# Kernel optimization log

Measured on AMD Instinct MI355X. Metric: run time of the kernel, lower is better.

## Reference

```python
import jax, jax.numpy as jnp
import numpy as np

SD = 64      # state_dim
EMO = 16     # emo_dim
D = SD + EMO # fractal node dim
C = SD       # quantum in/out channels
E = SD * 5   # MHA embed dim (320)
NH = 4       # MHA heads
HD = E // NH
F = D * 5    # flattened fractal node state
LIGHT = 500.0


def setup_inputs() -> dict:
    key = jax.random.key(0)
    ks = iter(jax.random.split(key, 48))
    def n(shape, s=0.02):
        return jax.random.normal(next(ks), shape, dtype=jnp.float32) * s
    return dict(
        node_states=jax.random.normal(next(ks), (27, SD, 5), dtype=jnp.float32),
        hist_state=jax.random.normal(next(ks), (27, SD, 5), dtype=jnp.float32),
        # CausalDiscoveryLayer params
        granger_W=n((2 * SD * 5, 1)), granger_b=jnp.zeros((1,), jnp.float32),
        mha_in_W=n((3 * E, E)), mha_in_b=jnp.zeros((3 * E,), jnp.float32),
        mha_out_W=n((E, E)), mha_out_b=jnp.zeros((E,), jnp.float32),
        # QuantumEntangledGNN params
        q_real=n((27, C), 0.01), q_imag=n((27, C), 0.01),
        ent_W1=n((2 * C, 64)), ent_b1=jnp.zeros((64,), jnp.float32),
        ent_W2=n((64, C)), ent_b2=jnp.zeros((C,), jnp.float32),
        meas_W=n((2 * C, C * 5)), meas_b=jnp.zeros((C * 5,), jnp.float32),
        # FractalGNN (depth 2, 27-ary): 729 leaves, 27 mid, 1 root
        leaf_states=n((729, D, 5), 0.01),
        mid_states=n((27, D, 5), 0.01),
        root_state=n((D, 5), 0.01),
        mid_agg_W=n((27, 27 * F, F)), mid_agg_b=jnp.zeros((27, F), jnp.float32),
        root_agg_W=n((27 * F, F)), root_agg_b=jnp.zeros((F,), jnp.float32),
        mid_up_W1=n((27, 2 * F, 64)), mid_up_b1=jnp.zeros((27, 64), jnp.float32),
        mid_up_W2=n((27, 64, F)), mid_up_b2=jnp.zeros((27, F), jnp.float32),
        root_up_W1=n((2 * F, 64)), root_up_b1=jnp.zeros((64,), jnp.float32),
        root_up_W2=n((64, F)), root_up_b2=jnp.zeros((F,), jnp.float32),
    )


def _forward(node_states, hist_state, granger_W, granger_b, mha_in_W, mha_in_b,
             mha_out_W, mha_out_b, q_real, q_imag, ent_W1, ent_b1, ent_W2, ent_b2,
             meas_W, meas_b, leaf_states, mid_states, root_state, mid_agg_W,
             mid_agg_b, root_agg_W, root_agg_b, mid_up_W1, mid_up_b1, mid_up_W2,
             mid_up_b2, root_up_W1, root_up_b1, root_up_W2, root_up_b2):
    # ---- CausalDiscoveryLayer ----
    h = hist_state.reshape(27, SD * 5)   # historical_states[-1][j].view(-1)
    x = node_states.reshape(27, SD * 5)  # node_states[i].view(-1)
    # pred_input[i, j] = cat(hist[j], node[i]) -> granger test, all 27x27 pairs
    pred = jnp.concatenate([
        jnp.broadcast_to(h[None, :, :], (27, 27, SD * 5)),
        jnp.broadcast_to(x[:, None, :], (27, 27, SD * 5))], axis=-1)
    scores = jax.nn.sigmoid(pred @ granger_W + granger_b)[..., 0]
    # .item() in original detaches -> stop_gradient; diagonal stays zero
    causal_adj = jax.lax.stop_gradient(scores * (1.0 - jnp.eye(27, dtype=scores.dtype)))
    hertz_w = jnp.clip(jnp.float32(LIGHT / 1000.0), 0.1, 1.0)
    qkv = x @ mha_in_W.T + mha_in_b
    q, k, v = jnp.split(qkv, 3, axis=-1)
    qh = q.reshape(27, NH, HD).transpose(1, 0, 2)  # [h, s, d]
    kh = k.reshape(27, NH, HD).transpose(1, 0, 2)
    vh = v.reshape(27, NH, HD).transpose(1, 0, 2)
    attn = jax.nn.softmax(jnp.einsum('hqd,hkd->hqk', qh, kh) / jnp.float32(HD) ** 0.5, axis=-1)
    o = jnp.einsum('hqk,hkd->hqd', attn, vh).transpose(1, 0, 2).reshape(27, E)
    attended = ((o @ mha_out_W.T + mha_out_b) * hertz_w).reshape(27, SD, 5)

    # ---- QuantumEntangledGNN (351 unordered pairs i<j) ----
    iu, ju = np.triu_indices(27, 1)
    comb = jnp.concatenate([q_real[iu], q_real[ju]], axis=-1)       # [351, 2C]
    ent = jax.nn.relu(comb @ ent_W1 + ent_b1) @ ent_W2 + ent_b2     # [351, C]
    s = q_real.sum(axis=1)
    coupling = jnp.exp(-jnp.abs(s[iu] - s[ju]) / (LIGHT + 1e-6))
    avg_ent = (ent * coupling[:, None]).mean(axis=0)                # [C]
    qr = q_real + avg_ent[None, :]
    qi = q_imag + avg_ent[None, :]
    measured = (jnp.concatenate([qr, qi], axis=-1) @ meas_W + meas_b).reshape(3, 3, 3, C, 5)

    # ---- FractalGNN: leaves are passthrough; 27 mid nodes update, then root ----
    child_flat = leaf_states.reshape(27, 27 * F)  # each mid node's 27 leaf children
    agg = jnp.einsum('nij,ni->nj', mid_agg_W, child_flat) + mid_agg_b  # [27, F]
    comb_m = jnp.concatenate([mid_states.reshape(27, F), agg], axis=-1)
    hid = jax.nn.relu(jnp.einsum('nij,ni->nj', mid_up_W1, comb_m) + mid_up_b1)
    upd = jnp.einsum('nij,ni->nj', mid_up_W2, hid) + mid_up_b2
    new_mid = mid_states + upd.reshape(27, D, 5)
    cf = new_mid.reshape(27 * F)
    agg_r = cf @ root_agg_W + root_agg_b
    comb_r = jnp.concatenate([root_state.reshape(F), agg_r], axis=-1)
    new_root = root_state + (jax.nn.relu(comb_r @ root_up_W1 + root_up_b1) @ root_up_W2 + root_up_b2).reshape(D, 5)

    return causal_adj, attended, measured, new_root


def reference(node_states, hist_state, granger_W, granger_b, mha_in_W, mha_in_b,
              mha_out_W, mha_out_b, q_real, q_imag, ent_W1, ent_b1, ent_W2, ent_b2,
              meas_W, meas_b, leaf_states, mid_states, root_state, mid_agg_W,
              mid_agg_b, root_agg_W, root_agg_b, mid_up_W1, mid_up_b1, mid_up_W2,
              mid_up_b2, root_up_W1, root_up_b1, root_up_W2, root_up_b2):
    return _forward(node_states, hist_state, granger_W, granger_b, mha_in_W,
                    mha_in_b, mha_out_W, mha_out_b, q_real, q_imag, ent_W1, ent_b1,
                    ent_W2, ent_b2, meas_W, meas_b, leaf_states, mid_states,
                    root_state, mid_agg_W, mid_agg_b, root_agg_W, root_agg_b,
                    mid_up_W1, mid_up_b1, mid_up_W2, mid_up_b2, root_up_W1,
                    root_up_b1, root_up_W2, root_up_b2)
```

## Files before the change

kernel.cpp:

```cpp
#include <hip/hip_runtime.h>
#include <math.h>

typedef float v4f __attribute__((ext_vector_type(4)));

#define SD 64
#define CC 64
#define EE 320
#define NS 27
#define NPAIR 351

#define NCHUNK 54
#define AGG_BLKS (27 * NCHUNK)

#define WS_QKV   0
#define WS_ENT   25920
#define WS_MIDP  48384
#define WS_CF    1214784
#define WS_ROOTP 1225584
#define WS_HPM   1268784
#define WS_HPR   1275696
#define WS_CTR   1275968


__device__ void dev_mid_agg(int blk, const float* __restrict__ W,
                            const float* __restrict__ leaf, float* __restrict__ partial) {
    __shared__ float c_l[200];
    int n = blk / NCHUNK, chunk = blk % NCHUNK;
    int t = threadIdx.x;
    if (t < 200) c_l[t] = leaf[n * 10800 + chunk * 200 + t];
    __syncthreads();
    if (t < 200) {
        int rp = t / 100, j4 = t % 100;
        const v4f* Wr = (const v4f*)(W + (size_t)(n * 10800 + chunk * 200) * 400);
        v4f acc = (v4f)(0.0f);
        #pragma unroll 16
        for (int rr = 0; rr < 100; ++rr) {
            int r = 2 * rr + rp;
            v4f w = __builtin_nontemporal_load(&Wr[(size_t)r * 100 + j4]);
            acc += c_l[r] * w;
        }
        ((v4f*)(partial + (size_t)(blk * 2 + rp) * 400))[j4] = acc;
    }
}

__device__ void dev_granger(int blk, const float* __restrict__ x, const float* __restrict__ h,
                            const float* __restrict__ gW, const float* __restrict__ gb,
                            float* __restrict__ out) {
    int idx = blk * 256 + threadIdx.x;
    if (idx >= NS * NS) return;
    int i = idx / NS, j = idx % NS;
    const float* hr = h + j * 320;
    const float* xr = x + i * 320;
    float acc = gb[0];
    for (int k = 0; k < 320; ++k) acc += hr[k] * gW[k] + xr[k] * gW[320 + k];
    float sig = 1.0f / (1.0f + expf(-acc));
    out[idx] = (i == j) ? 0.0f : sig;
}

__device__ void dev_qkv(int blk, const float* __restrict__ x, const float* __restrict__ W,
                        const float* __restrict__ b, float* __restrict__ qkv) {
    int idx = blk * 256 + threadIdx.x;
    if (idx >= NS * 960) return;
    int i = idx / 960, c = idx % 960;
    const float4* xr = (const float4*)(x + i * 320);
    const float4* wr = (const float4*)(W + (size_t)c * 320);
    float acc = b[c];
    #pragma unroll 8
    for (int k = 0; k < 80; ++k) {
        float4 a = xr[k], w = wr[k];
        acc += a.x * w.x + a.y * w.y + a.z * w.z + a.w * w.w;
    }
    qkv[idx] = acc;
}

__device__ void dev_ent(int blk, const float* __restrict__ q_real,
                        const float* __restrict__ W1, const float* __restrict__ b1,
                        const float* __restrict__ W2, const float* __restrict__ b2,
                        float* __restrict__ ent_scaled) {
    __shared__ float comb[2][128];
    __shared__ float hid[2][64];
    int t = threadIdx.x;
    int sub = t >> 7, lt = t & 127;
    int p = blk * 2 + sub;
    bool pv = (p < NPAIR);
    bool valid = pv && (lt < 64);
    int i = 0, jj = 0;
    if (pv) {
        int rem = p;
        while (rem >= 26 - i) { rem -= 26 - i; ++i; }
        jj = i + 1 + rem;
    }
    float qa = 0.f, qb = 0.f;
    if (valid) { qa = q_real[i * CC + lt]; qb = q_real[jj * CC + lt]; }
    float sa = qa, sb = qb;
    #pragma unroll
    for (int off = 32; off; off >>= 1) { sa += __shfl_xor(sa, off); sb += __shfl_xor(sb, off); }
    float coupling = expf(-fabsf(sa - sb) / (500.0f + 1e-6f));
    if (valid) { comb[sub][lt] = qa; comb[sub][64 + lt] = qb; }
    __syncthreads();
    if (valid) {
        float hs = b1[lt];
        for (int ii = 0; ii < 128; ++ii) hs += comb[sub][ii] * W1[ii * 64 + lt];
        hid[sub][lt] = fmaxf(hs, 0.0f);
    }
    __syncthreads();
    if (valid) {
        float e = b2[lt];
        for (int k = 0; k < 64; ++k) e += hid[sub][k] * W2[k * 64 + lt];
        ent_scaled[p * 64 + lt] = e * coupling;
    }
}

__global__ __launch_bounds__(256) void k_stage1(
    const float* __restrict__ mid_agg_W, const float* __restrict__ leaf,
    const float* __restrict__ node, const float* __restrict__ hist,
    const float* __restrict__ gW, const float* __restrict__ gb,
    const float* __restrict__ mha_in_W, const float* __restrict__ mha_in_b,
    const float* __restrict__ q_real,
    const float* __restrict__ ent_W1, const float* __restrict__ ent_b1,
    const float* __restrict__ ent_W2, const float* __restrict__ ent_b2,
    float* __restrict__ mid_partial, float* __restrict__ out_causal,
    float* __restrict__ qkv, float* __restrict__ ent_scaled,
    int* __restrict__ ctrs) {
    int blk = blockIdx.x;
    if (blk == 0 && threadIdx.x >= 224) ctrs[threadIdx.x - 224] = 0;
    if (blk < AGG_BLKS)            dev_mid_agg(blk, mid_agg_W, leaf, mid_partial);
    else if (blk < AGG_BLKS + 3)   dev_granger(blk - AGG_BLKS, node, hist, gW, gb, out_causal);
    else if (blk < AGG_BLKS + 105) dev_qkv(blk - AGG_BLKS - 3, node, mha_in_W, mha_in_b, qkv);
    else                           dev_ent(blk - AGG_BLKS - 105, q_real, ent_W1, ent_b1, ent_W2, ent_b2, ent_scaled);
}


__device__ void dev_attn(int blk, const float* __restrict__ qkv, float* __restrict__ o) {
    int h = blk / NS, q = blk % NS;
    int t = threadIdx.x;
    __shared__ float sc[NS];
    __shared__ float at[NS];
    if (t < NS) {
        const float* qrow = qkv + q * 960 + h * 80;
        const float* krow = qkv + t * 960 + EE + h * 80;
        float s = 0.0f;
        for (int d = 0; d < 80; ++d) s += qrow[d] * krow[d];
        sc[t] = s * 0.1118033988749895f;
    }
    __syncthreads();
    if (t < NS) {
        float m = -1e30f;
        for (int s2 = 0; s2 < NS; ++s2) m = fmaxf(m, sc[s2]);
        float sum = 0.0f;
        for (int s2 = 0; s2 < NS; ++s2) sum += expf(sc[s2] - m);
        at[t] = expf(sc[t] - m) / sum;
    }
    __syncthreads();
    if (t < 80) {
        float acc = 0.0f;
        for (int s2 = 0; s2 < NS; ++s2) acc += at[s2] * qkv[s2 * 960 + 2 * EE + h * 80 + t];
        o[q * EE + h * 80 + t] = acc;
    }
}

__device__ void dev_avg(const float* __restrict__ ent_scaled, float* __restrict__ avg) {
    __shared__ float aacc[8][64];
    int t = threadIdx.x;
    int col = t & 63, grp = t >> 6;
    float s = 0.0f;
    for (int p = grp; p < NPAIR; p += 8) s += ent_scaled[p * 64 + col];
    aacc[grp][col] = s;
    __syncthreads();
    if (t < 64) {
        float a = 0.0f;
        #pragma unroll
        for (int g = 0; g < 8; ++g) a += aacc[g][t];
        avg[t] = a / (float)NPAIR;
    }
}

__device__ void dev_mid_up(int rel, const float* __restrict__ partial, const float* __restrict__ agg_b,
                           const float* __restrict__ mid_states,
                           const float* __restrict__ W1, const float* __restrict__ b1,
                           const float* __restrict__ W2, const float* __restrict__ b2,
                           float* __restrict__ cf, float* __restrict__ hpm, int* __restrict__ ctrs) {
    int n = rel >> 2, p = rel & 3;
    __shared__ float combq[200];
    __shared__ float hp8[8][64];
    __shared__ float hid[64];
    __shared__ int flag;
    int t = threadIdx.x;
    if (p < 2) {
        if (t < 200) combq[t] = mid_states[n * 400 + p * 200 + t];
    } else {
        int j0 = (p - 2) * 200;
        if (t < 200) {
            float a = agg_b[n * 400 + j0 + t];
            const float* pp = partial + (size_t)(n * 108) * 400 + j0 + t;
            #pragma unroll 12
            for (int s = 0; s < 108; ++s) a += pp[s * 400];
            combq[t] = a;
        }
    }
    __syncthreads();
    {
        int h = t & 63, g = t >> 6;
        const float* w1 = W1 + (size_t)n * 51200 + (size_t)(p * 200) * 64;
        float hs = 0.0f;
        #pragma unroll 5
        for (int i = g * 25; i < g * 25 + 25; ++i) hs += combq[i] * w1[i * 64 + h];
        hp8[g][h] = hs;
    }
    __syncthreads();
    if (t < 64) {
        float hs = 0.0f;
        #pragma unroll
        for (int g = 0; g < 8; ++g) hs += hp8[g][t];
        hpm[(n * 4 + p) * 64 + t] = hs;
    }
    __syncthreads();
    if (t == 0) {
        int old = __hip_atomic_fetch_add(&ctrs[n], 1, __ATOMIC_ACQ_REL, __HIP_MEMORY_SCOPE_AGENT);
        flag = (old == 3);
    }
    __syncthreads();
    if (flag) {
        if (t < 64) {
            float hs = b1[n * 64 + t];
            #pragma unroll
            for (int pq = 0; pq < 4; ++pq) hs += hpm[(n * 4 + pq) * 64 + t];
            hid[t] = fmaxf(hs, 0.0f);
        }
        __syncthreads();
        const float* w2 = W2 + (size_t)n * 25600;
        if (t < 400) {
            float u = b2[n * 400 + t];
            #pragma unroll 8
            for (int k = 0; k < 64; ++k) u += hid[k] * w2[k * 400 + t];
            cf[n * 400 + t] = mid_states[n * 400 + t] + u;
        }
    }
}

__global__ __launch_bounds__(512) void k_stage2(
    const float* __restrict__ qkv, float* __restrict__ o,
    const float* __restrict__ ent_scaled, float* __restrict__ avg,
    const float* __restrict__ mid_partial, const float* __restrict__ mid_agg_b,
    const float* __restrict__ mid_states,
    const float* __restrict__ mid_up_W1, const float* __restrict__ mid_up_b1,
    const float* __restrict__ mid_up_W2, const float* __restrict__ mid_up_b2,
    float* __restrict__ cf, float* __restrict__ hpm, int* __restrict__ ctrs) {
    int blk = blockIdx.x;
    if (blk < 108)       dev_attn(blk, qkv, o);
    else if (blk == 108) dev_avg(ent_scaled, avg);
    else                 dev_mid_up(blk - 109, mid_partial, mid_agg_b, mid_states,
                                    mid_up_W1, mid_up_b1, mid_up_W2, mid_up_b2, cf, hpm, ctrs);
}


__device__ void dev_proj(int blk, const float* __restrict__ o, const float* __restrict__ W,
                         const float* __restrict__ b, float* __restrict__ outp) {
    int idx = blk * 512 + threadIdx.x;
    if (idx >= NS * EE) return;
    int i = idx / EE, c = idx % EE;
    const float4* orow = (const float4*)(o + i * EE);
    const float4* wr = (const float4*)(W + (size_t)c * EE);
    float acc = b[c];
    #pragma unroll 8
    for (int k = 0; k < 80; ++k) {
        float4 a = orow[k], w = wr[k];
        acc += a.x * w.x + a.y * w.y + a.z * w.z + a.w * w.w;
    }
    outp[idx] = 0.5f * acc;
}

__device__ void dev_measured(int blk, const float* __restrict__ q_real, const float* __restrict__ q_imag,
                             const float* __restrict__ avg, const float* __restrict__ W,
                             const float* __restrict__ b, float* __restrict__ out) {
    int idx = blk * 512 + threadIdx.x;
    if (idx >= NS * EE) return;
    int i = idx / EE, c = idx % EE;
    float acc = b[c];
    #pragma unroll 8
    for (int k = 0; k < 64; ++k) {
        float a = avg[k];
        acc += (q_real[i * 64 + k] + a) * W[k * EE + c];
        acc += (q_imag[i * 64 + k] + a) * W[(64 + k) * EE + c];
    }
    out[idx] = acc;
}

__device__ void dev_rootagg(int chunk, const float* __restrict__ W, const float* __restrict__ cf,
                            float* __restrict__ partial_r) {
    __shared__ float racc[5][400];
    int t = threadIdx.x;
    int rp = t / 100, j4 = t % 100;
    if (rp < 5) {
        const float* c = cf + chunk * 100;
        const v4f* Wr = (const v4f*)W + (size_t)(chunk * 100) * 100;
        v4f acc = (v4f)(0.0f);
        #pragma unroll
        for (int rr = 0; rr < 20; ++rr) {
            int r = 5 * rr + rp;
            float cv = c[r];
            v4f w = __builtin_nontemporal_load(&Wr[(size_t)r * 100 + j4]);
            acc += cv * w;
        }
        racc[rp][j4 * 4 + 0] = acc.x;
        racc[rp][j4 * 4 + 1] = acc.y;
        racc[rp][j4 * 4 + 2] = acc.z;
        racc[rp][j4 * 4 + 3] = acc.w;
    }
    __syncthreads();
    if (t < 400) {
        float a = 0.0f;
        #pragma unroll
        for (int g = 0; g < 5; ++g) a += racc[g][t];
        partial_r[chunk * 400 + t] = a;
    }
}

__global__ __launch_bounds__(512) void k_stage3(
    const float* __restrict__ o, const float* __restrict__ mha_out_W,
    const float* __restrict__ mha_out_b, float* __restrict__ out_att,
    const float* __restrict__ q_real, const float* __restrict__ q_imag,
    const float* __restrict__ avg, const float* __restrict__ meas_W,
    const float* __restrict__ meas_b, float* __restrict__ out_meas,
    const float* __restrict__ root_agg_W, const float* __restrict__ cf,
    float* __restrict__ partial_r) {
    int blk = blockIdx.x;
    if (blk < 17)       dev_proj(blk, o, mha_out_W, mha_out_b, out_att);
    else if (blk < 34)  dev_measured(blk - 17, q_real, q_imag, avg, meas_W, meas_b, out_meas);
    else                dev_rootagg(blk - 34, root_agg_W, cf, partial_r);
}

__global__ __launch_bounds__(512) void k_root(
    const float* __restrict__ partial_r, const float* __restrict__ agg_b,
    const float* __restrict__ root_state,
    const float* __restrict__ W1, const float* __restrict__ b1,
    const float* __restrict__ W2, const float* __restrict__ b2,
    float* __restrict__ out, float* __restrict__ hpr, int* __restrict__ ctrs) {
    int qd = blockIdx.x;
    __shared__ float combq[200];
    __shared__ float hp8[8][64];
    __shared__ float hid[64];
    __shared__ int flag;
    int t = threadIdx.x;
    if (qd < 2) {
        if (t < 200) combq[t] = root_state[qd * 200 + t];
    } else {
        int j0 = (qd - 2) * 200;
        if (t < 200) {
            float a = agg_b[j0 + t];
            const float* pp = partial_r + j0 + t;
            #pragma unroll 12
            for (int s = 0; s < 108; ++s) a += pp[s * 400];
            combq[t] = a;
        }
    }
    __syncthreads();
    {
        int h = t & 63, g = t >> 6;
        const float* w1 = W1 + (size_t)(qd * 200) * 64;
        float hs = 0.0f;
        #pragma unroll 5
        for (int i = g * 25; i < g * 25 + 25; ++i) hs += combq[i] * w1[i * 64 + h];
        hp8[g][h] = hs;
    }
    __syncthreads();
    if (t < 64) {
        float hs = 0.0f;
        #pragma unroll
        for (int g = 0; g < 8; ++g) hs += hp8[g][t];
        hpr[qd * 64 + t] = hs;
    }
    __syncthreads();
    if (t == 0) {
        int old = __hip_atomic_fetch_add(&ctrs[30], 1, __ATOMIC_ACQ_REL, __HIP_MEMORY_SCOPE_AGENT);
        flag = (old == 3);
    }
    __syncthreads();
    if (flag) {
        if (t < 64) {
            float hs = b1[t];
            #pragma unroll
            for (int pq = 0; pq < 4; ++pq) hs += hpr[pq * 64 + t];
            hid[t] = fmaxf(hs, 0.0f);
        }
        __syncthreads();
        if (t < 400) {
            float u = b2[t];
            #pragma unroll 8
            for (int k = 0; k < 64; ++k) u += hid[k] * W2[k * 400 + t];
            out[t] = root_state[t] + u;
        }
    }
}

extern "C" void kernel_launch(void* const* d_in, const int* in_sizes, int n_in,
                              void* d_out, int out_size, void* d_ws, size_t ws_size,
                              hipStream_t stream) {
    const float* node       = (const float*)d_in[0];
    const float* hist       = (const float*)d_in[1];
    const float* gW         = (const float*)d_in[2];
    const float* gb         = (const float*)d_in[3];
    const float* mha_in_W   = (const float*)d_in[4];
    const float* mha_in_b   = (const float*)d_in[5];
    const float* mha_out_W  = (const float*)d_in[6];
    const float* mha_out_b  = (const float*)d_in[7];
    const float* q_real     = (const float*)d_in[8];
    const float* q_imag     = (const float*)d_in[9];
    const float* ent_W1     = (const float*)d_in[10];
    const float* ent_b1     = (const float*)d_in[11];
    const float* ent_W2     = (const float*)d_in[12];
    const float* ent_b2     = (const float*)d_in[13];
    const float* meas_W     = (const float*)d_in[14];
    const float* meas_b     = (const float*)d_in[15];
    const float* leaf       = (const float*)d_in[16];
    const float* mid_states = (const float*)d_in[17];
    const float* root_state = (const float*)d_in[18];
    const float* mid_agg_W  = (const float*)d_in[19];
    const float* mid_agg_b  = (const float*)d_in[20];
    const float* root_agg_W = (const float*)d_in[21];
    const float* root_agg_b = (const float*)d_in[22];
    const float* mid_up_W1  = (const float*)d_in[23];
    const float* mid_up_b1  = (const float*)d_in[24];
    const float* mid_up_W2  = (const float*)d_in[25];
    const float* mid_up_b2  = (const float*)d_in[26];
    const float* root_up_W1 = (const float*)d_in[27];
    const float* root_up_b1 = (const float*)d_in[28];
    const float* root_up_W2 = (const float*)d_in[29];
    const float* root_up_b2 = (const float*)d_in[30];

    float* ws          = (float*)d_ws;
    float* qkv         = ws + WS_QKV;
    float* ent_scaled  = ws + WS_ENT;
    float* mid_partial = ws + WS_MIDP;
    float* cf          = ws + WS_CF;
    float* partial_r   = ws + WS_ROOTP;
    float* hpm         = ws + WS_HPM;
    float* hpr         = ws + WS_HPR;
    int*   ctrs        = (int*)(ws + WS_CTR);

    float* o = ws + WS_CTR + 32;

    float* out        = (float*)d_out;
    float* out_causal = out;
    float* out_att    = out + 729;
    float* out_meas   = out + 9369;
    float* out_root   = out + 18009;

    float* avg = o + 8640;

    hipLaunchKernelGGL(k_stage1, dim3(AGG_BLKS + 105 + 176), dim3(256), 0, stream,
                       mid_agg_W, leaf, node, hist, gW, gb, mha_in_W, mha_in_b,
                       q_real, ent_W1, ent_b1, ent_W2, ent_b2,
                       mid_partial, out_causal, qkv, ent_scaled, ctrs);

    hipLaunchKernelGGL(k_stage2, dim3(217), dim3(512), 0, stream,
                       qkv, o, ent_scaled, avg, mid_partial, mid_agg_b, mid_states,
                       mid_up_W1, mid_up_b1, mid_up_W2, mid_up_b2, cf, hpm, ctrs);

    hipLaunchKernelGGL(k_stage3, dim3(142), dim3(512), 0, stream,
                       o, mha_out_W, mha_out_b, out_att,
                       q_real, q_imag, avg, meas_W, meas_b, out_meas,
                       root_agg_W, cf, partial_r);

    hipLaunchKernelGGL(k_root, dim3(4), dim3(512), 0, stream,
                       partial_r, root_agg_b, root_state,
                       root_up_W1, root_up_b1, root_up_W2, root_up_b2, out_root, hpr, ctrs);
}
```

Baseline: 141.8 us.

## Fuse root update into stage3 via last-block atomic and enlarge agg blocks

Stage1 now runs 512-thread blocks: each mid_agg block covers 400 leaf rows with 5 row-groups reduced in shared memory, halving chunk count and shrinking the partial buffer that stage2 has to sum. Granger, QKV and entanglement blocks are re-indexed for the 512-thread size. The separate k_root launch is removed; the last finishing rootagg block, chosen via an atomic counter, does the root MLP. This cuts one kernel launch and partial traffic, but serializes the root MLP onto a single block.

```diff
diff --git a/kernel.cpp b/kernel.cpp
--- a/kernel.cpp
+++ b/kernel.cpp
@@ -9,44 +9,51 @@
 #define NS 27
 #define NPAIR 351
 
-#define NCHUNK 54
+#define NCHUNK 27
 #define AGG_BLKS (27 * NCHUNK)
 
 #define WS_QKV   0
 #define WS_ENT   25920
 #define WS_MIDP  48384
-#define WS_CF    1214784
-#define WS_ROOTP 1225584
-#define WS_HPM   1268784
-#define WS_HPR   1275696
-#define WS_CTR   1275968
+#define WS_CF    339984
+#define WS_ROOTP 350784
+#define WS_HPM   393984
+#define WS_CTR   400896
+#define WS_O     400928
+#define WS_AVG   409568
 
 
 __device__ void dev_mid_agg(int blk, const float* __restrict__ W,
                             const float* __restrict__ leaf, float* __restrict__ partial) {
-    __shared__ float c_l[200];
+    __shared__ float c_l[400];
+    __shared__ __align__(16) float racc[5][400];
     int n = blk / NCHUNK, chunk = blk % NCHUNK;
     int t = threadIdx.x;
-    if (t < 200) c_l[t] = leaf[n * 10800 + chunk * 200 + t];
-    __syncthreads();
-    if (t < 200) {
+    if (t < 400) c_l[t] = leaf[n * 10800 + chunk * 400 + t];
+    __syncthreads();
+    if (t < 500) {
         int rp = t / 100, j4 = t % 100;
-        const v4f* Wr = (const v4f*)(W + (size_t)(n * 10800 + chunk * 200) * 400);
+        const v4f* Wr = (const v4f*)(W + (size_t)(n * 10800 + chunk * 400) * 400);
         v4f acc = (v4f)(0.0f);
-        #pragma unroll 16
-        for (int rr = 0; rr < 100; ++rr) {
-            int r = 2 * rr + rp;
+        #pragma unroll 10
+        for (int rr = 0; rr < 80; ++rr) {
+            int r = 5 * rr + rp;
             v4f w = __builtin_nontemporal_load(&Wr[(size_t)r * 100 + j4]);
             acc += c_l[r] * w;
         }
-        ((v4f*)(partial + (size_t)(blk * 2 + rp) * 400))[j4] = acc;
+        ((v4f*)&racc[rp][0])[j4] = acc;
+    }
+    __syncthreads();
+    if (t < 400) {
+        float a = racc[0][t] + racc[1][t] + racc[2][t] + racc[3][t] + racc[4][t];
+        partial[(size_t)blk * 400 + t] = a;
     }
 }
 
 __device__ void dev_granger(int blk, const float* __restrict__ x, const float* __restrict__ h,
                             const float* __restrict__ gW, const float* __restrict__ gb,
                             float* __restrict__ out) {
-    int idx = blk * 256 + threadIdx.x;
+    int idx = blk * 512 + threadIdx.x;
     if (idx >= NS * NS) return;
     int i = idx / NS, j = idx % NS;
     const float* hr = h + j * 320;
@@ -59,7 +66,7 @@
 
 __device__ void dev_qkv(int blk, const float* __restrict__ x, const float* __restrict__ W,
                         const float* __restrict__ b, float* __restrict__ qkv) {
-    int idx = blk * 256 + threadIdx.x;
+    int idx = blk * 512 + threadIdx.x;
     if (idx >= NS * 960) return;
     int i = idx / 960, c = idx % 960;
     const float4* xr = (const float4*)(x + i * 320);
@@ -77,11 +84,11 @@
                         const float* __restrict__ W1, const float* __restrict__ b1,
                         const float* __restrict__ W2, const float* __restrict__ b2,
                         float* __restrict__ ent_scaled) {
-    __shared__ float comb[2][128];
-    __shared__ float hid[2][64];
+    __shared__ float comb[4][128];
+    __shared__ float hid[4][64];
     int t = threadIdx.x;
     int sub = t >> 7, lt = t & 127;
-    int p = blk * 2 + sub;
+    int p = blk * 4 + sub;
     bool pv = (p < NPAIR);
     bool valid = pv && (lt < 64);
     int i = 0, jj = 0;
@@ -111,7 +118,7 @@
     }
 }
 
-__global__ __launch_bounds__(256) void k_stage1(
+__global__ __launch_bounds__(512) void k_stage1(
     const float* __restrict__ mid_agg_W, const float* __restrict__ leaf,
     const float* __restrict__ node, const float* __restrict__ hist,
     const float* __restrict__ gW, const float* __restrict__ gb,
@@ -123,11 +130,11 @@
     float* __restrict__ qkv, float* __restrict__ ent_scaled,
     int* __restrict__ ctrs) {
     int blk = blockIdx.x;
-    if (blk == 0 && threadIdx.x >= 224) ctrs[threadIdx.x - 224] = 0;
-    if (blk < AGG_BLKS)            dev_mid_agg(blk, mid_agg_W, leaf, mid_partial);
-    else if (blk < AGG_BLKS + 3)   dev_granger(blk - AGG_BLKS, node, hist, gW, gb, out_causal);
-    else if (blk < AGG_BLKS + 105) dev_qkv(blk - AGG_BLKS - 3, node, mha_in_W, mha_in_b, qkv);
-    else                           dev_ent(blk - AGG_BLKS - 105, q_real, ent_W1, ent_b1, ent_W2, ent_b2, ent_scaled);
+    if (blk == 0 && threadIdx.x >= 480) ctrs[threadIdx.x - 480] = 0;
+    if (blk < AGG_BLKS)           dev_mid_agg(blk, mid_agg_W, leaf, mid_partial);
+    else if (blk < AGG_BLKS + 2)  dev_granger(blk - AGG_BLKS, node, hist, gW, gb, out_causal);
+    else if (blk < AGG_BLKS + 53) dev_qkv(blk - AGG_BLKS - 2, node, mha_in_W, mha_in_b, qkv);
+    else                          dev_ent(blk - AGG_BLKS - 53, q_real, ent_W1, ent_b1, ent_W2, ent_b2, ent_scaled);
 }
 
 
@@ -192,9 +199,9 @@
         int j0 = (p - 2) * 200;
         if (t < 200) {
             float a = agg_b[n * 400 + j0 + t];
-            const float* pp = partial + (size_t)(n * 108) * 400 + j0 + t;
-            #pragma unroll 12
-            for (int s = 0; s < 108; ++s) a += pp[s * 400];
+            const float* pp = partial + (size_t)(n * NCHUNK) * 400 + j0 + t;
+            #pragma unroll 9
+            for (int s = 0; s < NCHUNK; ++s) a += pp[s * 400];
             combq[t] = a;
         }
     }
@@ -287,32 +294,80 @@
 }
 
 __device__ void dev_rootagg(int chunk, const float* __restrict__ W, const float* __restrict__ cf,
-                            float* __restrict__ partial_r) {
-    __shared__ float racc[5][400];
-    int t = threadIdx.x;
-    int rp = t / 100, j4 = t % 100;
-    if (rp < 5) {
-        const float* c = cf + chunk * 100;
+                            float* __restrict__ partial_r,
+                            const float* __restrict__ agg_b, const float* __restrict__ root_state,
+                            const float* __restrict__ W1, const float* __restrict__ b1,
+                            const float* __restrict__ W2, const float* __restrict__ b2,
+                            float* __restrict__ out, int* __restrict__ ctrs) {
+    __shared__ float c_l[100];
+    __shared__ __align__(16) float racc[5][400];
+    __shared__ int flag;
+    int t = threadIdx.x;
+    if (t < 100) c_l[t] = cf[chunk * 100 + t];
+    __syncthreads();
+    if (t < 500) {
+        int rp = t / 100, j4 = t % 100;
         const v4f* Wr = (const v4f*)W + (size_t)(chunk * 100) * 100;
         v4f acc = (v4f)(0.0f);
         #pragma unroll
         for (int rr = 0; rr < 20; ++rr) {
             int r = 5 * rr + rp;
-            float cv = c[r];
             v4f w = __builtin_nontemporal_load(&Wr[(size_t)r * 100 + j4]);
-            acc += cv * w;
-        }
-        racc[rp][j4 * 4 + 0] = acc.x;
-        racc[rp][j4 * 4 + 1] = acc.y;
-        racc[rp][j4 * 4 + 2] = acc.z;
-        racc[rp][j4 * 4 + 3] = acc.w;
+            acc += c_l[r] * w;
+        }
+        ((v4f*)&racc[rp][0])[j4] = acc;
     }
     __syncthreads();
     if (t < 400) {
-        float a = 0.0f;
+        float a = racc[0][t] + racc[1][t] + racc[2][t] + racc[3][t] + racc[4][t];
+        partial_r[chunk * 400 + t] = a;
+    }
+    __syncthreads();
+    if (t == 0) {
+        int old = __hip_atomic_fetch_add(&ctrs[31], 1, __ATOMIC_ACQ_REL, __HIP_MEMORY_SCOPE_AGENT);
+        flag = (old == 107);
+    }
+    __syncthreads();
+    if (!flag) return;
+
+    __shared__ float comb[800];
+    __shared__ __align__(16) float s4f[2048];
+    __shared__ float hid[64];
+    if (t < 400) {
+        float a = agg_b[t];
+        const float* pp = partial_r + t;
+        #pragma unroll 12
+        for (int s = 0; s < 108; ++s) a += pp[s * 400];
+        comb[400 + t] = a;
+        comb[t] = root_state[t];
+    }
+    __syncthreads();
+    {
+        const float4* W1f = (const float4*)W1;
+        int i0 = t >> 4;
+        float4 a4 = make_float4(0.f, 0.f, 0.f, 0.f);
         #pragma unroll
-        for (int g = 0; g < 5; ++g) a += racc[g][t];
-        partial_r[chunk * 400 + t] = a;
+        for (int it = 0; it < 25; ++it) {
+            float4 w = W1f[t + 512 * it];
+            float cv = comb[i0 + 32 * it];
+            a4.x += cv * w.x; a4.y += cv * w.y; a4.z += cv * w.z; a4.w += cv * w.w;
+        }
+        ((float4*)s4f)[t] = a4;
+    }
+    __syncthreads();
+    if (t < 64) {
+        float hs = b1[t];
+        int r = t >> 2, c = t & 3;
+        #pragma unroll 8
+        for (int g = 0; g < 32; ++g) hs += s4f[(r + 16 * g) * 4 + c];
+        hid[t] = fmaxf(hs, 0.0f);
+    }
+    __syncthreads();
+    if (t < 400) {
+        float u = b2[t];
+        #pragma unroll 8
+        for (int k = 0; k < 64; ++k) u += hid[k] * W2[k * 400 + t];
+        out[t] = root_state[t] + u;
     }
 }
 
@@ -323,74 +378,17 @@
     const float* __restrict__ avg, const float* __restrict__ meas_W,
     const float* __restrict__ meas_b, float* __restrict__ out_meas,
     const float* __restrict__ root_agg_W, const float* __restrict__ cf,
-    float* __restrict__ partial_r) {
+    float* __restrict__ partial_r,
+    const float* __restrict__ root_agg_b, const float* __restrict__ root_state,
+    const float* __restrict__ root_up_W1, const float* __restrict__ root_up_b1,
+    const float* __restrict__ root_up_W2, const float* __restrict__ root_up_b2,
+    float* __restrict__ out_root, int* __restrict__ ctrs) {
     int blk = blockIdx.x;
     if (blk < 17)       dev_proj(blk, o, mha_out_W, mha_out_b, out_att);
     else if (blk < 34)  dev_measured(blk - 17, q_real, q_imag, avg, meas_W, meas_b, out_meas);
-    else                dev_rootagg(blk - 34, root_agg_W, cf, partial_r);
-}
-
-__global__ __launch_bounds__(512) void k_root(
-    const float* __restrict__ partial_r, const float* __restrict__ agg_b,
-    const float* __restrict__ root_state,
-    const float* __restrict__ W1, const float* __restrict__ b1,
-    const float* __restrict__ W2, const float* __restrict__ b2,
-    float* __restrict__ out, float* __restrict__ hpr, int* __restrict__ ctrs) {
-    int qd = blockIdx.x;
-    __shared__ float combq[200];
-    __shared__ float hp8[8][64];
-    __shared__ float hid[64];
-    __shared__ int flag;
-    int t = threadIdx.x;
-    if (qd < 2) {
-        if (t < 200) combq[t] = root_state[qd * 200 + t];
-    } else {
-        int j0 = (qd - 2) * 200;
-        if (t < 200) {
-            float a = agg_b[j0 + t];
-            const float* pp = partial_r + j0 + t;
-            #pragma unroll 12
-            for (int s = 0; s < 108; ++s) a += pp[s * 400];
-            combq[t] = a;
-        }
-    }
-    __syncthreads();
-    {
-        int h = t & 63, g = t >> 6;
-        const float* w1 = W1 + (size_t)(qd * 200) * 64;
-        float hs = 0.0f;
-        #pragma unroll 5
-        for (int i = g * 25; i < g * 25 + 25; ++i) hs += combq[i] * w1[i * 64 + h];
-        hp8[g][h] = hs;
-    }
-    __syncthreads();
-    if (t < 64) {
-        float hs = 0.0f;
-        #pragma unroll
-        for (int g = 0; g < 8; ++g) hs += hp8[g][t];
-        hpr[qd * 64 + t] = hs;
-    }
-    __syncthreads();
-    if (t == 0) {
-        int old = __hip_atomic_fetch_add(&ctrs[30], 1, __ATOMIC_ACQ_REL, __HIP_MEMORY_SCOPE_AGENT);
-        flag = (old == 3);
-    }
-    __syncthreads();
-    if (flag) {
-        if (t < 64) {
-            float hs = b1[t];
-            #pragma unroll
-            for (int pq = 0; pq < 4; ++pq) hs += hpr[pq * 64 + t];
-            hid[t] = fmaxf(hs, 0.0f);
-        }
-        __syncthreads();
-        if (t < 400) {
-            float u = b2[t];
-            #pragma unroll 8
-            for (int k = 0; k < 64; ++k) u += hid[k] * W2[k * 400 + t];
-            out[t] = root_state[t] + u;
-        }
-    }
+    else                dev_rootagg(blk - 34, root_agg_W, cf, partial_r,
+                                    root_agg_b, root_state, root_up_W1, root_up_b1,
+                                    root_up_W2, root_up_b2, out_root, ctrs);
 }
 
 extern "C" void kernel_launch(void* const* d_in, const int* in_sizes, int n_in,
@@ -435,10 +433,9 @@
     float* cf          = ws + WS_CF;
     float* partial_r   = ws + WS_ROOTP;
     float* hpm         = ws + WS_HPM;
-    float* hpr         = ws + WS_HPR;
     int*   ctrs        = (int*)(ws + WS_CTR);
-
-    float* o = ws + WS_CTR + 32;
+    float* o           = ws + WS_O;
+    float* avg         = ws + WS_AVG;
 
     float* out        = (float*)d_out;
     float* out_causal = out;
@@ -446,9 +443,7 @@
     float* out_meas   = out + 9369;
     float* out_root   = out + 18009;
 
-    float* avg = o + 8640;
-
-    hipLaunchKernelGGL(k_stage1, dim3(AGG_BLKS + 105 + 176), dim3(256), 0, stream,
+    hipLaunchKernelGGL(k_stage1, dim3(AGG_BLKS + 2 + 51 + 88), dim3(512), 0, stream,
                        mid_agg_W, leaf, node, hist, gW, gb, mha_in_W, mha_in_b,
                        q_real, ent_W1, ent_b1, ent_W2, ent_b2,
                        mid_partial, out_causal, qkv, ent_scaled, ctrs);
@@ -460,9 +455,7 @@
     hipLaunchKernelGGL(k_stage3, dim3(142), dim3(512), 0, stream,
                        o, mha_out_W, mha_out_b, out_att,
                        q_real, q_imag, avg, meas_W, meas_b, out_meas,
-                       root_agg_W, cf, partial_r);
-
-    hipLaunchKernelGGL(k_root, dim3(4), dim3(512), 0, stream,
-                       partial_r, root_agg_b, root_state,
-                       root_up_W1, root_up_b1, root_up_W2, root_up_b2, out_root, hpr, ctrs);
-}
+                       root_agg_W, cf, partial_r,
+                       root_agg_b, root_state, root_up_W1, root_up_b1,
+                       root_up_W2, root_up_b2, out_root, ctrs);
+}
```

Measured after the change: 144.7 us. 1.02x slower.
